# Kernel tuning notes

Measured on AMD Instinct MI355X. Metric: run time of the kernel, lower is better.

The kernel has to match this reference:

```python
import jax, jax.numpy as jnp
import numpy as np

CHANNELS = 8
IN_CHANNELS = 8
MASK_OUT_STRIDE = 4
WEIGHT_NUMS = [(IN_CHANNELS + 2) * CHANNELS, CHANNELS * CHANNELS, CHANNELS * 1]
BIAS_NUMS = [CHANNELS, CHANNELS, 1]
SOI = jnp.array([8.0, 16.0, 32.0, 64.0, 128.0], dtype=jnp.float32)
EPS = 1e-5


def compute_locations(h, w, stride):
    # (x, y) center of each stride-sized cell, row-major (y outer, x inner)
    sx = jnp.arange(w, dtype=jnp.float32) * stride + stride // 2
    sy = jnp.arange(h, dtype=jnp.float32) * stride + stride // 2
    yy, xx = jnp.meshgrid(sy, sx, indexing='ij')
    return jnp.stack([xx.reshape(-1), yy.reshape(-1)], axis=-1)  # [H*W, 2]


def aligned_bilinear(t, factor):
    # Matches AdelaiDet aligned_bilinear: replicate-pad right/bottom, bilinear
    # upsample align_corners=True to (f*h+1, f*w+1), replicate-pad top/left by
    # f//2, crop to (f*h, f*w).
    if factor == 1:
        return t
    n, c, h, w = t.shape
    t = jnp.pad(t, ((0, 0), (0, 0), (0, 1), (0, 1)), mode='edge')  # [n,c,h+1,w+1]
    oh, ow = factor * h + 1, factor * w + 1
    ys = jnp.arange(oh, dtype=jnp.float32) / factor  # align_corners mapping
    xs = jnp.arange(ow, dtype=jnp.float32) / factor
    y0 = jnp.floor(ys).astype(jnp.int32)
    x0 = jnp.floor(xs).astype(jnp.int32)
    y1 = jnp.minimum(y0 + 1, h)
    x1 = jnp.minimum(x0 + 1, w)
    wy = (ys - y0.astype(jnp.float32)).astype(t.dtype)
    wx = (xs - x0.astype(jnp.float32)).astype(t.dtype)
    ty = t[:, :, y0, :] * (1.0 - wy)[None, None, :, None] + t[:, :, y1, :] * wy[None, None, :, None]
    out = ty[:, :, :, x0] * (1.0 - wx) + ty[:, :, :, x1] * wx
    p = factor // 2
    out = jnp.pad(out, ((0, 0), (0, 0), (p, 0), (p, 0)), mode='edge')
    return out[:, :, :oh - 1, :ow - 1]


def parse_dynamic_params(params):
    n = params.shape[0]
    splits = jnp.split(params, np.cumsum(WEIGHT_NUMS + BIAS_NUMS)[:-1], axis=1)
    w0 = splits[0].reshape(n, CHANNELS, IN_CHANNELS + 2)
    w1 = splits[1].reshape(n, CHANNELS, CHANNELS)
    w2 = splits[2].reshape(n, 1, CHANNELS)
    b0 = splits[3].reshape(n, CHANNELS)
    b1 = splits[4].reshape(n, CHANNELS)
    b2 = splits[5].reshape(n, 1)
    return (w0, w1, w2), (b0, b1, b2)


def setup_inputs() -> dict:
    key = jax.random.key(0)
    ks = jax.random.split(key, 6)
    N, H, W = 2, 100, 136
    n_inst = 500
    return {
        'mask_feats': jax.random.normal(ks[0], (N, IN_CHANNELS, H, W), dtype=jnp.float32),
        'mask_head_params': jax.random.normal(ks[1], (n_inst, 169), dtype=jnp.float32),
        'locations_inst': jax.random.uniform(ks[2], (n_inst, 2), dtype=jnp.float32),
        'gt_bitmasks': jax.random.uniform(ks[3], (n_inst, 1, 2 * H, 2 * W), dtype=jnp.float32),
        'im_inds': jax.random.randint(ks[4], (n_inst,), 0, N, dtype=jnp.int64 if jax.config.jax_enable_x64 else jnp.int32),
        'fpn_levels': jax.random.randint(ks[5], (n_inst,), 0, 5, dtype=jnp.int64 if jax.config.jax_enable_x64 else jnp.int32),
        'mask_feat_stride': 8,
    }


def reference(mask_feats, mask_head_params, locations_inst, gt_bitmasks, im_inds, fpn_levels, mask_feat_stride):
    N, Cin, H, W = mask_feats.shape
    n = mask_head_params.shape[0]
    # relative coordinates, normalized by per-instance size-of-interest
    locs = compute_locations(H, W, mask_feat_stride)                 # [HW, 2]
    rel = locations_inst[:, None, :] - locs[None, :, :]              # [n, HW, 2]
    rel = jnp.transpose(rel, (0, 2, 1))                              # [n, 2, HW]
    soi = SOI[fpn_levels]                                            # [n]
    rel = (rel / soi[:, None, None]).astype(mask_feats.dtype)
    feats = mask_feats[im_inds].reshape(n, Cin, H * W)               # gather per instance
    x = jnp.concatenate([rel, feats], axis=1)                        # [n, Cin+2, HW]
    # per-instance 1x1 conv stack == batched small GEMMs
    (w0, w1, w2), (b0, b1, b2) = parse_dynamic_params(mask_head_params)
    x = jax.nn.relu(jnp.einsum('nci,nip->ncp', w0, x) + b0[:, :, None])
    x = jax.nn.relu(jnp.einsum('nci,nip->ncp', w1, x) + b1[:, :, None])
    x = jnp.einsum('nci,nip->ncp', w2, x) + b2[:, :, None]           # [n, 1, HW]
    logits = x.reshape(n, 1, H, W)
    logits = aligned_bilinear(logits, mask_feat_stride // MASK_OUT_STRIDE)
    scores = jax.nn.sigmoid(logits)                                  # [n, 1, 2H, 2W]
    # dice loss
    xs = scores.reshape(n, -1)
    t = gt_bitmasks.reshape(n, -1)
    inter = jnp.sum(xs * t, axis=1)
    union = jnp.sum(xs * xs, axis=1) + jnp.sum(t * t, axis=1) + EPS
    loss = 1.0 - 2.0 * inter / union
    return jnp.mean(loss)
```

## Files before the change

### kernel.cpp

```cpp
#include <hip/hip_runtime.h>
#include <hip/hip_bf16.h>
#include <math.h>

#define CIN      8
#define H_IN     100
#define W_IN     136
#define NPIX     (H_IN * W_IN)
#define OH       (2 * H_IN)
#define OW       (2 * W_IN)
#define ONPIX    (OH * OW)
#define NPARAMS  169
#define EPSV     1e-5f


__global__ __launch_bounds__(256, 2)
void mask_head_fused(const float* __restrict__ mask_feats,
                     const float* __restrict__ params,
                     const float* __restrict__ locs,
                     const float* __restrict__ gt,
                     const int*   __restrict__ im_inds,
                     const int*   __restrict__ fpn_levels,
                     float*       __restrict__ losses)
{
    const int inst = blockIdx.x;
    const int tid  = threadIdx.x;

    __shared__ float s_par[NPARAMS];
    __shared__ float s_logit[NPIX];
    __shared__ float s_red[12];

    if (tid < NPARAMS) s_par[tid] = params[inst * NPARAMS + tid];

    const int   im  = im_inds[inst];
    const int   lvl = fpn_levels[inst];
    const float inv_soi = exp2f(-(float)(3 + lvl));
    const float lx = locs[inst * 2 + 0];
    const float ly = locs[inst * 2 + 1];

    __syncthreads();

    const float* feat = mask_feats + (size_t)im * (CIN * NPIX);

    #pragma unroll 1
    for (int base = 0; base < NPIX; base += 1024) {
        const int p0 = base + tid;
        float in[10][4];
        #pragma unroll
        for (int k = 0; k < 4; ++k) {
            int p  = p0 + (k << 8);
            int pc = p < NPIX ? p : NPIX - 1;
            int y  = pc / W_IN;
            int x  = pc - y * W_IN;
            in[0][k] = (lx - (float)(x * 8 + 4)) * inv_soi;
            in[1][k] = (ly - (float)(y * 8 + 4)) * inv_soi;
            #pragma unroll
            for (int c = 0; c < CIN; ++c)
                in[2 + c][k] = feat[c * NPIX + pc];
        }

        float h0[8][4];
        #pragma unroll
        for (int o = 0; o < 8; ++o) {
            float b = s_par[152 + o];
            float a0 = b, a1 = b, a2 = b, a3 = b;
            #pragma unroll
            for (int i = 0; i < 10; ++i) {
                float w = s_par[o * 10 + i];
                a0 = fmaf(w, in[i][0], a0);
                a1 = fmaf(w, in[i][1], a1);
                a2 = fmaf(w, in[i][2], a2);
                a3 = fmaf(w, in[i][3], a3);
            }
            h0[o][0] = fmaxf(a0, 0.f);
            h0[o][1] = fmaxf(a1, 0.f);
            h0[o][2] = fmaxf(a2, 0.f);
            h0[o][3] = fmaxf(a3, 0.f);
        }

        float h1[8][4];
        #pragma unroll
        for (int o = 0; o < 8; ++o) {
            float b = s_par[160 + o];
            float a0 = b, a1 = b, a2 = b, a3 = b;
            #pragma unroll
            for (int i = 0; i < 8; ++i) {
                float w = s_par[80 + o * 8 + i];
                a0 = fmaf(w, h0[i][0], a0);
                a1 = fmaf(w, h0[i][1], a1);
                a2 = fmaf(w, h0[i][2], a2);
                a3 = fmaf(w, h0[i][3], a3);
            }
            h1[o][0] = fmaxf(a0, 0.f);
            h1[o][1] = fmaxf(a1, 0.f);
            h1[o][2] = fmaxf(a2, 0.f);
            h1[o][3] = fmaxf(a3, 0.f);
        }

        float b2 = s_par[168];
        float o0 = b2, o1 = b2, o2 = b2, o3 = b2;
        #pragma unroll
        for (int i = 0; i < 8; ++i) {
            float w = s_par[144 + i];
            o0 = fmaf(w, h1[i][0], o0);
            o1 = fmaf(w, h1[i][1], o1);
            o2 = fmaf(w, h1[i][2], o2);
            o3 = fmaf(w, h1[i][3], o3);
        }
        float outv[4] = {o0, o1, o2, o3};
        #pragma unroll
        for (int k = 0; k < 4; ++k) {
            int p = p0 + (k << 8);
            if (p < NPIX) s_logit[p] = outv[k];
        }
    }

    __syncthreads();

    float inter = 0.f, ssum = 0.f, tsum = 0.f;
    const float* gtp = gt + (size_t)inst * ONPIX;

    #pragma unroll 1
    for (int base = 0; base < ONPIX; base += 1024) {
        const int p = base + (tid << 2);
        if (p < ONPIX) {
            const float4 t4 = *(const float4*)(gtp + p);
            const float tv[4] = {t4.x, t4.y, t4.z, t4.w};
            const int oy  = p / OW;
            const int ox0 = p - oy * OW;
            const int sy  = oy > 0 ? oy - 1 : 0;
            const int y0  = sy >> 1;
            const float wy = (sy & 1) ? 0.5f : 0.f;
            const int y1  = (y0 + 1 < H_IN) ? y0 + 1 : H_IN - 1;
            const float* r0 = s_logit + y0 * W_IN;
            const float* r1 = s_logit + y1 * W_IN;
            #pragma unroll
            for (int j = 0; j < 4; ++j) {
                int ox = ox0 + j;
                int sx = ox > 0 ? ox - 1 : 0;
                int x0 = sx >> 1;
                float wx = (sx & 1) ? 0.5f : 0.f;
                int x1 = (x0 + 1 < W_IN) ? x0 + 1 : W_IN - 1;
                float a  = r0[x0], b = r0[x1];
                float c  = r1[x0], d = r1[x1];
                float top = a + wx * (b - a);
                float bot = c + wx * (d - c);
                float l   = top + wy * (bot - top);
                float s   = 1.f / (1.f + __expf(-l));
                float t   = tv[j];
                inter = fmaf(s, t, inter);
                ssum  = fmaf(s, s, ssum);
                tsum  = fmaf(t, t, tsum);
            }
        }
    }

    #pragma unroll
    for (int off = 32; off > 0; off >>= 1) {
        inter += __shfl_down(inter, off, 64);
        ssum  += __shfl_down(ssum,  off, 64);
        tsum  += __shfl_down(tsum,  off, 64);
    }
    const int wid = tid >> 6;
    if ((tid & 63) == 0) {
        s_red[wid * 3 + 0] = inter;
        s_red[wid * 3 + 1] = ssum;
        s_red[wid * 3 + 2] = tsum;
    }
    __syncthreads();
    if (tid == 0) {
        float I = 0.f, S = 0.f, T = 0.f;
        #pragma unroll
        for (int w = 0; w < 4; ++w) {
            I += s_red[w * 3 + 0];
            S += s_red[w * 3 + 1];
            T += s_red[w * 3 + 2];
        }
        float uni = S + T + EPSV;
        losses[inst] = 1.f - 2.f * I / uni;
    }
}

__global__ __launch_bounds__(512)
void loss_mean_kernel(const float* __restrict__ losses, float* __restrict__ out, int n)
{
    __shared__ float s_red[8];
    float v = 0.f;
    for (int i = threadIdx.x; i < n; i += 512) v += losses[i];
    #pragma unroll
    for (int off = 32; off > 0; off >>= 1) v += __shfl_down(v, off, 64);
    const int wid = threadIdx.x >> 6;
    if ((threadIdx.x & 63) == 0) s_red[wid] = v;
    __syncthreads();
    if (threadIdx.x == 0) {
        float s = 0.f;
        #pragma unroll
        for (int w = 0; w < 8; ++w) s += s_red[w];
        out[0] = s / (float)n;
    }
}

extern "C" void kernel_launch(void* const* d_in, const int* in_sizes, int n_in,
                              void* d_out, int out_size, void* d_ws, size_t ws_size,
                              hipStream_t stream)
{
    const float* mask_feats = (const float*)d_in[0];
    const float* params     = (const float*)d_in[1];
    const float* locs       = (const float*)d_in[2];
    const float* gt         = (const float*)d_in[3];
    const int*   im_inds    = (const int*)d_in[4];
    const int*   fpn_levels = (const int*)d_in[5];

    const int n = in_sizes[4];
    float* losses = (float*)d_ws;

    mask_head_fused<<<n, 256, 0, stream>>>(mask_feats, params, locs, gt,
                                           im_inds, fpn_levels, losses);
    loss_mean_kernel<<<1, 512, 0, stream>>>(losses, (float*)d_out, n);
}
```

Measured before the change: 218.4 us.

## Split each instance into four row slices with specialized 2x upsample and partial reduction

Each instance's work is split across four blocks, each covering 25 low-res rows plus one halo row. This shrinks shared memory per block and raises occupancy, with launch bounds going from 2 to 4 blocks per CU. The upsample/dice stage now treats each low-res row pair as one task, using closed-form half-weight interpolation, vectorized gt loads and a fast reciprocal sigmoid. Per-slice partial sums are combined in the final kernel. The cost is recomputing halo rows and four times as many blocks, each reloading the parameters.

```diff
diff --git a/kernel.cpp b/kernel.cpp
--- a/kernel.cpp
+++ b/kernel.cpp
@@ -11,22 +11,37 @@
 #define ONPIX    (OH * OW)
 #define NPARAMS  169
 #define EPSV     1e-5f
-
-
-__global__ __launch_bounds__(256, 2)
+#define NSLICE   4
+#define PAIRS_PER_SLICE 25
+#define KGROUPS  34
+#define TASKS    (PAIRS_PER_SLICE * KGROUPS)
+
+
+__device__ __forceinline__ float sigmoidf_fast(float x) {
+    float e = __expf(-x);
+    return __builtin_amdgcn_rcpf(1.f + e);
+}
+
+__global__ __launch_bounds__(256, 4)
 void mask_head_fused(const float* __restrict__ mask_feats,
                      const float* __restrict__ params,
                      const float* __restrict__ locs,
                      const float* __restrict__ gt,
                      const int*   __restrict__ im_inds,
                      const int*   __restrict__ fpn_levels,
-                     float*       __restrict__ losses)
+                     float*       __restrict__ partials)
 {
-    const int inst = blockIdx.x;
-    const int tid  = threadIdx.x;
+    const int inst  = blockIdx.x >> 2;
+    const int slice = blockIdx.x & 3;
+    const int tid   = threadIdx.x;
+
+    const int r_start = (slice == 0) ? 0 : 25 * slice - 1;
+    const int r_end   = 25 * slice + 24;
+    const int nrows   = r_end - r_start + 1;
+    const int npx     = nrows * W_IN;
 
     __shared__ float s_par[NPARAMS];
-    __shared__ float s_logit[NPIX];
+    __shared__ float s_logit[26 * W_IN];
     __shared__ float s_red[12];
 
     if (tid < NPARAMS) s_par[tid] = params[inst * NPARAMS + tid];
@@ -40,22 +55,25 @@
     __syncthreads();
 
     const float* feat = mask_feats + (size_t)im * (CIN * NPIX);
+    const int goff = r_start * W_IN;
 
     #pragma unroll 1
-    for (int base = 0; base < NPIX; base += 1024) {
+    for (int base = 0; base < 26 * W_IN; base += 1024) {
         const int p0 = base + tid;
         float in[10][4];
         #pragma unroll
         for (int k = 0; k < 4; ++k) {
             int p  = p0 + (k << 8);
-            int pc = p < NPIX ? p : NPIX - 1;
-            int y  = pc / W_IN;
-            int x  = pc - y * W_IN;
+            int pc = p < npx ? p : npx - 1;
+            int r  = pc / W_IN;
+            int x  = pc - r * W_IN;
+            int y  = r_start + r;
             in[0][k] = (lx - (float)(x * 8 + 4)) * inv_soi;
             in[1][k] = (ly - (float)(y * 8 + 4)) * inv_soi;
+            int gp = goff + pc;
             #pragma unroll
             for (int c = 0; c < CIN; ++c)
-                in[2 + c][k] = feat[c * NPIX + pc];
+                in[2 + c][k] = feat[c * NPIX + gp];
         }
 
         float h0[8][4];
@@ -110,7 +128,7 @@
         #pragma unroll
         for (int k = 0; k < 4; ++k) {
             int p = p0 + (k << 8);
-            if (p < NPIX) s_logit[p] = outv[k];
+            if (p < npx) s_logit[p] = outv[k];
         }
     }
 
@@ -118,35 +136,60 @@
 
     float inter = 0.f, ssum = 0.f, tsum = 0.f;
     const float* gtp = gt + (size_t)inst * ONPIX;
+    const int pair_base = 25 * slice;
 
     #pragma unroll 1
-    for (int base = 0; base < ONPIX; base += 1024) {
-        const int p = base + (tid << 2);
-        if (p < ONPIX) {
-            const float4 t4 = *(const float4*)(gtp + p);
-            const float tv[4] = {t4.x, t4.y, t4.z, t4.w};
-            const int oy  = p / OW;
-            const int ox0 = p - oy * OW;
-            const int sy  = oy > 0 ? oy - 1 : 0;
-            const int y0  = sy >> 1;
-            const float wy = (sy & 1) ? 0.5f : 0.f;
-            const int y1  = (y0 + 1 < H_IN) ? y0 + 1 : H_IN - 1;
-            const float* r0 = s_logit + y0 * W_IN;
-            const float* r1 = s_logit + y1 * W_IN;
+    for (int base = 0; base < TASKS; base += 256) {
+        const int task = base + tid;
+        if (task < TASKS) {
+            const int pl = task / KGROUPS;
+            const int k  = task - pl * KGROUPS;
+            const int pg = pair_base + pl;
+            const int er = pg - r_start;
+            const int pr = (pg > 0 ? pg - 1 : 0) - r_start;
+            const float* E = s_logit + er * W_IN;
+            const float* P = s_logit + pr * W_IN;
+            const int c0  = 4 * k;
+            const int cm1 = (k > 0) ? c0 - 1 : 0;
+
+            const float4 e4 = *(const float4*)(E + c0);
+            const float  em = E[cm1];
+            const float4 p4 = *(const float4*)(P + c0);
+            const float  pm = P[cm1];
+
+            float Se[5] = {em, e4.x, e4.y, e4.z, e4.w};
+            float Sa[5] = {0.5f * (em + pm), 0.5f * (e4.x + p4.x), 0.5f * (e4.y + p4.y),
+                           0.5f * (e4.z + p4.z), 0.5f * (e4.w + p4.w)};
+
+            float oa[8], oe[8];
             #pragma unroll
             for (int j = 0; j < 4; ++j) {
-                int ox = ox0 + j;
-                int sx = ox > 0 ? ox - 1 : 0;
-                int x0 = sx >> 1;
-                float wx = (sx & 1) ? 0.5f : 0.f;
-                int x1 = (x0 + 1 < W_IN) ? x0 + 1 : W_IN - 1;
-                float a  = r0[x0], b = r0[x1];
-                float c  = r1[x0], d = r1[x1];
-                float top = a + wx * (b - a);
-                float bot = c + wx * (d - c);
-                float l   = top + wy * (bot - top);
-                float s   = 1.f / (1.f + __expf(-l));
-                float t   = tv[j];
+                oa[2 * j]     = 0.5f * (Sa[j] + Sa[j + 1]);
+                oa[2 * j + 1] = Sa[j + 1];
+                oe[2 * j]     = 0.5f * (Se[j] + Se[j + 1]);
+                oe[2 * j + 1] = Se[j + 1];
+            }
+
+            const float* g0 = gtp + (size_t)(2 * pg) * OW + 8 * k;
+            const float4 ga = *(const float4*)(g0);
+            const float4 gb = *(const float4*)(g0 + 4);
+            const float4 gc = *(const float4*)(g0 + OW);
+            const float4 gd = *(const float4*)(g0 + OW + 4);
+            const float tva[8] = {ga.x, ga.y, ga.z, ga.w, gb.x, gb.y, gb.z, gb.w};
+            const float tve[8] = {gc.x, gc.y, gc.z, gc.w, gd.x, gd.y, gd.z, gd.w};
+
+            #pragma unroll
+            for (int j = 0; j < 8; ++j) {
+                float s = sigmoidf_fast(oa[j]);
+                float t = tva[j];
+                inter = fmaf(s, t, inter);
+                ssum  = fmaf(s, s, ssum);
+                tsum  = fmaf(t, t, tsum);
+            }
+            #pragma unroll
+            for (int j = 0; j < 8; ++j) {
+                float s = sigmoidf_fast(oe[j]);
+                float t = tve[j];
                 inter = fmaf(s, t, inter);
                 ssum  = fmaf(s, s, ssum);
                 tsum  = fmaf(t, t, tsum);
@@ -175,17 +218,28 @@
             S += s_red[w * 3 + 1];
             T += s_red[w * 3 + 2];
         }
-        float uni = S + T + EPSV;
-        losses[inst] = 1.f - 2.f * I / uni;
+        partials[blockIdx.x * 3 + 0] = I;
+        partials[blockIdx.x * 3 + 1] = S;
+        partials[blockIdx.x * 3 + 2] = T;
     }
 }
 
 __global__ __launch_bounds__(512)
-void loss_mean_kernel(const float* __restrict__ losses, float* __restrict__ out, int n)
+void loss_mean_kernel(const float* __restrict__ partials, float* __restrict__ out, int n)
 {
     __shared__ float s_red[8];
     float v = 0.f;
-    for (int i = threadIdx.x; i < n; i += 512) v += losses[i];
+    for (int i = threadIdx.x; i < n; i += 512) {
+        float I = 0.f, S = 0.f, T = 0.f;
+        #pragma unroll
+        for (int s = 0; s < NSLICE; ++s) {
+            const float* p = partials + (size_t)(i * NSLICE + s) * 3;
+            I += p[0];
+            S += p[1];
+            T += p[2];
+        }
+        v += 1.f - 2.f * I / (S + T + EPSV);
+    }
     #pragma unroll
     for (int off = 32; off > 0; off >>= 1) v += __shfl_down(v, off, 64);
     const int wid = threadIdx.x >> 6;
@@ -211,9 +265,9 @@
     const int*   fpn_levels = (const int*)d_in[5];
 
     const int n = in_sizes[4];
-    float* losses = (float*)d_ws;
-
-    mask_head_fused<<<n, 256, 0, stream>>>(mask_feats, params, locs, gt,
-                                           im_inds, fpn_levels, losses);
-    loss_mean_kernel<<<1, 512, 0, stream>>>(losses, (float*)d_out, n);
-}
+    float* partials = (float*)d_ws;
+
+    mask_head_fused<<<n * NSLICE, 256, 0, stream>>>(mask_feats, params, locs, gt,
+                                                    im_inds, fpn_levels, partials);
+    loss_mean_kernel<<<1, 512, 0, stream>>>(partials, (float*)d_out, n);
+}
```

Result: slower. 637.8 us (+192.1%).
